# Kernel optimization log

Measured on AMD Instinct MI355X. Metric: run time of the kernel, lower is better.

## Reference

```python
import jax, jax.numpy as jnp
import numpy as np

B, S, H = 2, 2048, 2048           # batch, seq_len, hidden_size
NH, HD = 16, 128                  # num_heads, head_dim
ROPE_THETA = 10000.0


def _rope_cos_sin(seq_len, head_dim, dtype):
    # standard rotary embedding tables: [seq, head_dim]
    inv_freq = 1.0 / (ROPE_THETA ** (jnp.arange(0, head_dim, 2, dtype=jnp.float32) / head_dim))
    t = jnp.arange(seq_len, dtype=jnp.float32)
    freqs = jnp.einsum('s,d->sd', t, inv_freq)          # [S, HD/2]
    emb = jnp.concatenate([freqs, freqs], axis=-1)      # [S, HD]
    return jnp.cos(emb).astype(dtype), jnp.sin(emb).astype(dtype)


def _rotate_half(x):
    x1, x2 = jnp.split(x, 2, axis=-1)
    return jnp.concatenate([-x2, x1], axis=-1)


def _apply_rope(x, cos, sin):
    # x: [B, S, NH, HD]; cos/sin: [S, HD]
    return x * cos[None, :, None, :] + _rotate_half(x) * sin[None, :, None, :]


def setup_inputs() -> dict:
    key = jax.random.key(0)
    ks = jax.random.split(key, 10)
    hidden_states = jax.random.normal(ks[0], (B, S, H), dtype=jnp.float32)
    # causal mask: 1.0 where attention is disallowed (k > q), matching mask * -1e9 usage
    mask = jnp.triu(jnp.ones((S, S), dtype=jnp.float32), k=1)[None, None, :, :]
    mask = jnp.broadcast_to(mask, (B, 1, S, S))
    xav = 1.0 / np.sqrt(H)
    Wq = jax.random.uniform(ks[1], (H, NH, HD), jnp.float32, -xav, xav)
    Wk = jax.random.uniform(ks[2], (H, NH, HD), jnp.float32, -xav, xav)
    Wv = jax.random.uniform(ks[3], (H, NH, HD), jnp.float32, -xav, xav)
    Wo = jax.random.uniform(ks[4], (NH, HD, H), jnp.float32, -xav, xav)
    bq = jnp.zeros((NH, HD), jnp.float32)
    bk = jnp.zeros((NH, HD), jnp.float32)
    bv = jnp.zeros((NH, HD), jnp.float32)
    bo = jnp.zeros((H,), jnp.float32)
    return {"hidden_states": hidden_states, "mask": mask, "Wq": Wq, "bq": bq,
            "Wk": Wk, "bk": bk, "Wv": Wv, "bv": bv, "Wo": Wo, "bo": bo}


def reference(hidden_states, mask, Wq, bq, Wk, bk, Wv, bv, Wo, bo):
    dtype = hidden_states.dtype
    scale = 1.0 / jnp.sqrt(jnp.asarray(HD, dtype))
    # q/k/v projections: DenseGeneral hidden -> (heads, head_dim)
    q = jnp.einsum('bsh,bhd->bsnd'.replace('bhd', 'hnd'), hidden_states, Wq) + bq  # [B,S,NH,HD]
    k = jnp.einsum('bsh,hnd->bsnd', hidden_states, Wk) + bk
    v = jnp.einsum('bsh,hnd->bsnd', hidden_states, Wv) + bv
    cos, sin = _rope_cos_sin(hidden_states.shape[1], HD, dtype)
    q = _apply_rope(q, cos, sin)
    k = _apply_rope(k, cos, sin)
    # [B,NH,S,HD]
    q, k, v = (x.transpose(0, 2, 1, 3) for x in (q, k, v))
    attn_scores = jnp.einsum('bhqd,bhkd->bhqk', q, k) * scale
    attn_scores = attn_scores + mask * (-1e9)           # mask broadcasts over heads
    probs = jax.nn.softmax(attn_scores, axis=-1)
    attn_output = jnp.einsum('bhqk,bhkd->bhqd', probs, v)
    attn_output = attn_output.transpose(0, 2, 1, 3)      # [B,S,NH,HD]
    return jnp.einsum('bsnd,ndh->bsh', attn_output, Wo) + bo
```

## Files before the change

kernel.cpp:

```cpp
#include <hip/hip_runtime.h>
#include <hip/hip_bf16.h>

#define B_ 2
#define S_ 2048
#define H_ 2048
#define NH_ 16
#define HD_ 128
#define M_ (B_*S_)

typedef unsigned short u16;
typedef unsigned int u32;
typedef __attribute__((ext_vector_type(8))) short bhalf8_t;
typedef __attribute__((ext_vector_type(4))) float fx4_t;

__device__ __forceinline__ float bf2f(u16 v) {
    unsigned u = ((unsigned)v) << 16;
    return __builtin_bit_cast(float, u);
}
__device__ __forceinline__ u16 f2bf(float f) {
    unsigned u = __builtin_bit_cast(unsigned, f);
    unsigned r = u + 0x7fffu + ((u >> 16) & 1u);
    return (u16)(r >> 16);
}
__device__ __forceinline__ u16 f2bf_trunc(float f) {
    return (u16)(__builtin_bit_cast(unsigned, f) >> 16);
}
__device__ __forceinline__ void gload_lds16(const u16* g, u16* l) {
    __builtin_amdgcn_global_load_lds(
        (const __attribute__((address_space(1))) u32*)g,
        (__attribute__((address_space(3))) u32*)l, 16, 0, 0);
}
#define ASM_BAR()    __asm__ volatile("s_barrier" ::: "memory")
#define WAIT_VM0()   __asm__ volatile("s_waitcnt vmcnt(0)" ::: "memory")
#define WAIT_VM6()   __asm__ volatile("s_waitcnt vmcnt(6)" ::: "memory")
#define WAIT_LGKM0() __asm__ volatile("s_waitcnt lgkmcnt(0)" ::: "memory")

__global__ __launch_bounds__(256) void cvt_bf16_k(const float* __restrict__ in,
                                                  u16* __restrict__ out) {
    int i = blockIdx.x * 256 + threadIdx.x;
    float4 v = ((const float4*)in)[i];
    ushort4 o;
    o.x = f2bf(v.x); o.y = f2bf(v.y); o.z = f2bf(v.z); o.w = f2bf(v.w);
    ((ushort4*)out)[i] = o;
}

__global__ __launch_bounds__(256) void transpose_cvt4_k(const float* __restrict__ s0,
                                                        const float* __restrict__ s1,
                                                        const float* __restrict__ s2,
                                                        const float* __restrict__ s3,
                                                        u16* __restrict__ out) {
    const float* in = blockIdx.z == 0 ? s0 : blockIdx.z == 1 ? s1
                    : blockIdx.z == 2 ? s2 : s3;
    u16* dst = out + (size_t)blockIdx.z * H_ * H_;
    __shared__ u16 tile[64][65];
    int k0 = blockIdx.y * 64, n0 = blockIdx.x * 64;
    int t = threadIdx.x;
    for (int i = 0; i < 16; i++) {
        int idx = t + i * 256;
        int r = idx >> 6, c = idx & 63;
        tile[r][c] = f2bf(in[(size_t)(k0 + r) * H_ + n0 + c]);
    }
    __syncthreads();
    for (int i = 0; i < 16; i++) {
        int idx = t + i * 256;
        int r = idx >> 6, c = idx & 63;
        dst[(size_t)(n0 + r) * H_ + k0 + c] = tile[c][r];
    }
}

__global__ __launch_bounds__(512, 2) void gemm_qkv_tb(const u16* __restrict__ A,
                                                      const u16* __restrict__ Bt,
                                                      const float* __restrict__ bq,
                                                      const float* __restrict__ bk,
                                                      const float* __restrict__ bv,
                                                      u16* __restrict__ qh,
                                                      u16* __restrict__ kh,
                                                      u16* __restrict__ vT) {
    const int Ksz = H_;
    __shared__ u16 smA[3 * 8192];
    __shared__ u16 smB[3 * 16384];
    int t = threadIdx.x;
    int wave = t >> 6, lane = t & 63;
    int lr = lane & 15, lq = lane >> 4;
    int m0 = blockIdx.y * 128, n0 = blockIdx.x * 256;
    int wm = (wave >> 2) * 64, wn = (wave & 3) * 64;

    fx4_t acc[4][4];
#pragma unroll
    for (int i = 0; i < 4; i++)
        for (int j = 0; j < 4; j++)
            acc[i][j] = (fx4_t){0.f, 0.f, 0.f, 0.f};

    auto stageA = [&](int buf, int k0) {
        u16* dst = smA + buf * 8192;
#pragma unroll
        for (int i = 0; i < 2; i++) {
            int c = t + i * 512;
            int r = c >> 3, g = (c & 7) ^ (r & 7);
            gload_lds16(&A[(size_t)(m0 + r) * Ksz + k0 + g * 8], dst + (size_t)c * 8);
        }
    };
    auto stageB = [&](int buf, int k0) {
        u16* dst = smB + buf * 16384;
#pragma unroll
        for (int i = 0; i < 4; i++) {
            int c = t + i * 512;
            int r = c >> 3, g = (c & 7) ^ (r & 7);
            gload_lds16(&Bt[(size_t)(n0 + r) * Ksz + k0 + g * 8], dst + (size_t)c * 8);
        }
    };

    const int NT = Ksz / 64;
    stageA(0, 0);  stageB(0, 0);
    stageA(1, 64); stageB(1, 64);
    WAIT_VM6();
    ASM_BAR();

    for (int kt = 0; kt < NT; kt++) {
        int cur = kt % 3;
        const u16* Ab = smA + cur * 8192;
        const u16* Bb = smB + cur * 16384;
        bhalf8_t bfr[8];
        bhalf8_t afr[2][2];

#pragma unroll
        for (int nj = 0; nj < 4; nj++)
            for (int ks = 0; ks < 2; ks++) {
                int row = wn + nj * 16 + lr;
                bfr[nj * 2 + ks] = *(const bhalf8_t*)
                    &Bb[(((size_t)row << 3) + ((ks * 4 + lq) ^ (lr & 7))) * 8];
            }
#pragma unroll
        for (int mi2 = 0; mi2 < 2; mi2++)
            for (int ks = 0; ks < 2; ks++) {
                int row = wm + mi2 * 16 + lr;
                afr[mi2][ks] = *(const bhalf8_t*)
                    &Ab[(((size_t)row << 3) + ((ks * 4 + lq) ^ (lr & 7))) * 8];
            }
        if (kt + 2 < NT) {
            int nb = (kt + 2) % 3;
            stageA(nb, (kt + 2) * 64);
            stageB(nb, (kt + 2) * 64);
        }
        ASM_BAR();
        WAIT_LGKM0();
        __builtin_amdgcn_sched_barrier(0);
        __builtin_amdgcn_s_setprio(1);
#pragma unroll
        for (int mi2 = 0; mi2 < 2; mi2++)
            for (int nj = 0; nj < 4; nj++)
                for (int ks = 0; ks < 2; ks++)
                    acc[mi2][nj] = __builtin_amdgcn_mfma_f32_16x16x32_bf16(
                        afr[mi2][ks], bfr[nj * 2 + ks], acc[mi2][nj], 0, 0, 0);
        __builtin_amdgcn_s_setprio(0);
        ASM_BAR();

#pragma unroll
        for (int mi2 = 0; mi2 < 2; mi2++)
            for (int ks = 0; ks < 2; ks++) {
                int row = wm + (2 + mi2) * 16 + lr;
                afr[mi2][ks] = *(const bhalf8_t*)
                    &Ab[(((size_t)row << 3) + ((ks * 4 + lq) ^ (lr & 7))) * 8];
            }
        if (kt + 2 < NT) WAIT_VM6();
        else            WAIT_VM0();
        ASM_BAR();
        WAIT_LGKM0();
        __builtin_amdgcn_sched_barrier(0);
        __builtin_amdgcn_s_setprio(1);
#pragma unroll
        for (int mi2 = 0; mi2 < 2; mi2++)
            for (int nj = 0; nj < 4; nj++)
                for (int ks = 0; ks < 2; ks++)
                    acc[2 + mi2][nj] = __builtin_amdgcn_mfma_f32_16x16x32_bf16(
                        afr[mi2][ks], bfr[nj * 2 + ks], acc[2 + mi2][nj], 0, 0, 0);
        __builtin_amdgcn_s_setprio(0);
        ASM_BAR();
    }

    int which = n0 >> 11;
    const float* bias = which == 0 ? bq : which == 1 ? bk : bv;
#pragma unroll
    for (int mi = 0; mi < 4; mi++)
#pragma unroll
        for (int nj = 0; nj < 4; nj++) {
            int row0 = m0 + wm + mi * 16 + lq * 4;
            int cc = (n0 & 2047) + wn + nj * 16 + lr;
            float bvv = bias[cc];
            int bb = row0 >> 11, s = row0 & 2047;
            int hh = cc >> 7, d = cc & 127;
            if (which == 2) {
                ushort4 w;
                w.x = f2bf(acc[mi][nj][0] + bvv);
                w.y = f2bf(acc[mi][nj][1] + bvv);
                w.z = f2bf(acc[mi][nj][2] + bvv);
                w.w = f2bf(acc[mi][nj][3] + bvv);
                *(ushort4*)&vT[(((size_t)bb * NH_ + hh) * HD_ + d) * S_ + s] = w;
            } else {
                u16* dst = (which == 0 ? qh : kh);
                for (int r = 0; r < 4; r++)
                    dst[(((size_t)bb * NH_ + hh) * S_ + s + r) * HD_ + d] =
                        f2bf(acc[mi][nj][r] + bvv);
            }
        }
}

__global__ __launch_bounds__(256) void gemm_out(const u16* __restrict__ A,
                                                const u16* __restrict__ Bt,
                                                const float* __restrict__ bias,
                                                float* __restrict__ C) {
    const int Ksz = H_, Nsz = H_;
    __shared__ u16 As[128 * 64];
    __shared__ u16 Bs[128 * 64];
    int t = threadIdx.x;
    int wave = t >> 6, lane = t & 63;
    int lr = lane & 15, lq = lane >> 4;
    int m0 = blockIdx.y * 128, n0 = blockIdx.x * 128;
    int wm = (wave >> 1) * 64, wn = (wave & 1) * 64;

    fx4_t acc[4][4];
    for (int i = 0; i < 4; i++)
        for (int j = 0; j < 4; j++)
            acc[i][j] = (fx4_t){0.f, 0.f, 0.f, 0.f};

    for (int k0 = 0; k0 < Ksz; k0 += 64) {
        for (int i = 0; i < 4; i++) {
            int c = t + i * 256;
            int r = c >> 3, g = (c & 7) ^ (r & 7);
            gload_lds16(&A[(size_t)(m0 + r) * Ksz + k0 + g * 8], As + (size_t)c * 8);
            gload_lds16(&Bt[(size_t)(n0 + r) * Ksz + k0 + g * 8], Bs + (size_t)c * 8);
        }
        __syncthreads();
        for (int ds = 0; ds < 2; ds++) {
            bhalf8_t a[4], b[4];
            int cs = (ds * 4 + lq) ^ (lr & 7);
            for (int i = 0; i < 4; i++)
                a[i] = *(const bhalf8_t*)&As[(((wm + i * 16 + lr) << 3) + cs) * 8];
            for (int j = 0; j < 4; j++)
                b[j] = *(const bhalf8_t*)&Bs[(((wn + j * 16 + lr) << 3) + cs) * 8];
            for (int i = 0; i < 4; i++)
                for (int j = 0; j < 4; j++)
                    acc[i][j] = __builtin_amdgcn_mfma_f32_16x16x32_bf16(a[i], b[j], acc[i][j], 0, 0, 0);
        }
        __syncthreads();
    }
    for (int i = 0; i < 4; i++)
        for (int j = 0; j < 4; j++) {
            int row0 = m0 + wm + i * 16 + lq * 4;
            int col = n0 + wn + j * 16 + lr;
            float bvv = bias[col];
            for (int r = 0; r < 4; r++)
                C[(size_t)(row0 + r) * Nsz + col] = acc[i][j][r] + bvv;
        }
}

__global__ __launch_bounds__(256) void rope_k(u16* __restrict__ q, u16* __restrict__ k) {
    const float scale2 = 0.08838834764831845f * 1.44269504f;
    int idx = blockIdx.x * 256 + threadIdx.x;
    int i = idx & 63;
    int s = (idx >> 6) & 2047;
    int h = (idx >> 17) & 15;
    int b = idx >> 21;
    float inv = exp2f((float)i * (-13.287712379549449f / 64.0f));
    float ang = (float)s * inv;
    float sn, c;
    sincosf(ang, &sn, &c);
    size_t base = (((size_t)b * NH_ + h) * S_ + s) * HD_ + i;
    {
        float x1 = bf2f(q[base]), x2 = bf2f(q[base + 64]);
        q[base]      = f2bf((x1 * c - x2 * sn) * scale2);
        q[base + 64] = f2bf((x2 * c + x1 * sn) * scale2);
    }
    {
        float x1 = bf2f(k[base]), x2 = bf2f(k[base + 64]);
        k[base]      = f2bf(x1 * c - x2 * sn);
        k[base + 64] = f2bf(x2 * c + x1 * sn);
    }
}

#define PROW2 40
__global__ __launch_bounds__(256, 2) void flash_k(const u16* __restrict__ qh,
                                                  const u16* __restrict__ kh,
                                                  const u16* __restrict__ vT,
                                                  u16* __restrict__ attn) {
    __shared__ u16 sm[2 * 8192 + 2 * 8192 + 4 * 32 * PROW2];
    u16* KsB = sm;
    u16* VsB = sm + 16384;
    u16* Ps  = sm + 32768;

    int t = threadIdx.x, wave = t >> 6, lane = t & 63;
    int lr = lane & 15, lq = lane >> 4;
    int h = blockIdx.y, b = blockIdx.z;
    int ti = (b == 0) ? ((int)gridDim.x - 1 - (int)blockIdx.x) : (int)blockIdx.x;
    int q0 = ti * 128;

    const u16* kbase = kh + ((size_t)b * NH_ + h) * S_ * HD_;
    const u16* vbase = vT + ((size_t)b * NH_ + h) * HD_ * S_;
    u16* Pw = Ps + wave * 32 * PROW2;

    bhalf8_t aq[2][4];
#pragma unroll
    for (int rg = 0; rg < 2; rg++) {
        const u16* qrow =
            qh + (((size_t)b * NH_ + h) * S_ + q0 + wave * 32 + rg * 16 + lr) * HD_;
#pragma unroll
        for (int ds = 0; ds < 4; ds++)
            aq[rg][ds] = *(const bhalf8_t*)&qrow[ds * 32 + lq * 8];
    }

    float m_i[2][4], l_i[2][4];
    fx4_t acc_o[2][8];
#pragma unroll
    for (int rg = 0; rg < 2; rg++)
        for (int r = 0; r < 4; r++) { m_i[rg][r] = -INFINITY; l_i[rg][r] = 0.f; }
#pragma unroll
    for (int rg = 0; rg < 2; rg++)
        for (int dt = 0; dt < 8; dt++) acc_o[rg][dt] = (fx4_t){0.f, 0.f, 0.f, 0.f};

    bhalf8_t bones;
#pragma unroll
    for (int j = 0; j < 8; j++) bones[j] = (short)0x3F80;

    auto stageK = [&](int buf, int k0) {
        u16* dst = KsB + buf * 8192;
#pragma unroll
        for (int i = 0; i < 4; i++) {
            int c = t + i * 256;
            int r = c >> 4, g = (c & 15) ^ (r & 15);
            gload_lds16(&kbase[(size_t)(k0 + r) * HD_ + g * 8], dst + (size_t)c * 8);
        }
    };
    auto stageV = [&](int buf, int k0) {
        u16* dst = VsB + buf * 8192;
#pragma unroll
        for (int i = 0; i < 4; i++) {
            int c = t + i * 256;
            int r = c >> 3, g = (c & 7) ^ (r & 7);
            gload_lds16(&vbase[(size_t)r * S_ + k0 + g * 8], dst + (size_t)c * 8);
        }
    };

    int nkb = q0 / 64 + 2;
    stageK(0, 0);
    stageV(0, 0);
    for (int kbi = 0; kbi < nkb; kbi++) {
        int cur = kbi & 1;
        int k0 = kbi * 64;
        __syncthreads();
        if (kbi + 1 < nkb) {
            stageK(cur ^ 1, k0 + 64);
            stageV(cur ^ 1, k0 + 64);
        }
        const u16* Kc = KsB + cur * 8192;
        const u16* Vc = VsB + cur * 8192;

        bool active = (k0 <= q0 + wave * 32 + 31);

        fx4_t sacc[2][4];
        float alpha[2][4];
        if (active) {
#pragma unroll
            for (int rg = 0; rg < 2; rg++)
                for (int nt = 0; nt < 4; nt++)
                    sacc[rg][nt] = (fx4_t){0.f, 0.f, 0.f, 0.f};
            __builtin_amdgcn_s_setprio(1);
#pragma unroll
            for (int nt = 0; nt < 4; nt++) {
                int r = nt * 16 + lr;
#pragma unroll
                for (int ds = 0; ds < 4; ds++) {
                    bhalf8_t bk = *(const bhalf8_t*)&Kc[((r << 4) + ((ds * 4 + lq) ^ lr)) * 8];
                    sacc[0][nt] = __builtin_amdgcn_mfma_f32_16x16x32_bf16(aq[0][ds], bk, sacc[0][nt], 0, 0, 0);
                    sacc[1][nt] = __builtin_amdgcn_mfma_f32_16x16x32_bf16(aq[1][ds], bk, sacc[1][nt], 0, 0, 0);
                }
            }
            __builtin_amdgcn_s_setprio(0);

            if (kbi >= nkb - 2) {
#pragma unroll
                for (int rg = 0; rg < 2; rg++)
                    for (int nt = 0; nt < 4; nt++)
                        for (int r = 0; r < 4; r++) {
                            int kpos = k0 + nt * 16 + lr;
                            int qpos = q0 + wave * 32 + rg * 16 + lq * 4 + r;
                            if (kpos > qpos) sacc[rg][nt][r] = -1e30f;
                        }
            }

#pragma unroll
            for (int rg = 0; rg < 2; rg++) {
                float rmax[4];
#pragma unroll
                for (int r = 0; r < 4; r++)
                    rmax[r] = fmaxf(fmaxf(sacc[rg][0][r], sacc[rg][1][r]),
                                    fmaxf(sacc[rg][2][r], sacc[rg][3][r]));
#pragma unroll
                for (int off = 1; off < 16; off <<= 1)
                    for (int r = 0; r < 4; r++)
                        rmax[r] = fmaxf(rmax[r], __shfl_xor(rmax[r], off, 64));
#pragma unroll
                for (int r = 0; r < 4; r++) {
                    float mn = fmaxf(m_i[rg][r], rmax[r]);
                    alpha[rg][r] = exp2f(m_i[rg][r] - mn);
                    m_i[rg][r] = mn;
#pragma unroll
                    for (int nt = 0; nt < 4; nt++)
                        sacc[rg][nt][r] = exp2f(sacc[rg][nt][r] - mn);
                    l_i[rg][r] *= alpha[rg][r];
                }
#pragma unroll
                for (int dt = 0; dt < 8; dt++)
                    for (int r = 0; r < 4; r++) acc_o[rg][dt][r] *= alpha[rg][r];
            }

            fx4_t ls[2];
            ls[0] = (fx4_t){0.f, 0.f, 0.f, 0.f};
            ls[1] = (fx4_t){0.f, 0.f, 0.f, 0.f};
#pragma unroll
            for (int p = 0; p < 2; p++) {
#pragma unroll
                for (int rg = 0; rg < 2; rg++)
                    for (int nt2 = 0; nt2 < 2; nt2++)
                        for (int r = 0; r < 4; r++)
                            Pw[(rg * 16 + lq * 4 + r) * PROW2 + nt2 * 16 + lr] =
                                f2bf_trunc(sacc[rg][p * 2 + nt2][r]);
                __asm__ volatile("s_waitcnt lgkmcnt(0)" ::: "memory");
                bhalf8_t ap0 = *(const bhalf8_t*)&Pw[lr * PROW2 + lq * 8];
                bhalf8_t ap1 = *(const bhalf8_t*)&Pw[(16 + lr) * PROW2 + lq * 8];
                __builtin_amdgcn_s_setprio(1);
#pragma unroll
                for (int dt = 0; dt < 8; dt++) {
                    int r = dt * 16 + lr;
                    bhalf8_t bv = *(const bhalf8_t*)&Vc[((r << 3) + ((p * 4 + lq) ^ (lr & 7))) * 8];
                    acc_o[0][dt] = __builtin_amdgcn_mfma_f32_16x16x32_bf16(ap0, bv, acc_o[0][dt], 0, 0, 0);
                    acc_o[1][dt] = __builtin_amdgcn_mfma_f32_16x16x32_bf16(ap1, bv, acc_o[1][dt], 0, 0, 0);
                }
                ls[0] = __builtin_amdgcn_mfma_f32_16x16x32_bf16(ap0, bones, ls[0], 0, 0, 0);
                ls[1] = __builtin_amdgcn_mfma_f32_16x16x32_bf16(ap1, bones, ls[1], 0, 0, 0);
                __builtin_amdgcn_s_setprio(0);
            }
#pragma unroll
            for (int rg = 0; rg < 2; rg++)
                for (int r = 0; r < 4; r++) l_i[rg][r] += ls[rg][r];
        }
    }

#pragma unroll
    for (int rg = 0; rg < 2; rg++) {
        float rl[4];
#pragma unroll
        for (int r = 0; r < 4; r++) rl[r] = 1.f / l_i[rg][r];
#pragma unroll
        for (int dt = 0; dt < 8; dt++)
            for (int r = 0; r < 4; r++) {
                size_t row = (size_t)(b * S_ + q0 + wave * 32 + rg * 16 + lq * 4 + r);
                attn[(row * NH_ + h) * HD_ + dt * 16 + lr] = f2bf(acc_o[rg][dt][r] * rl[r]);
            }
    }
}

extern "C" void kernel_launch(void* const* d_in, const int* in_sizes, int n_in,
                              void* d_out, int out_size, void* d_ws, size_t ws_size,
                              hipStream_t stream) {
    const float* hs = (const float*)d_in[0];
    const float* Wq = (const float*)d_in[2];
    const float* bq = (const float*)d_in[3];
    const float* Wk = (const float*)d_in[4];
    const float* bk = (const float*)d_in[5];
    const float* Wv = (const float*)d_in[6];
    const float* bv = (const float*)d_in[7];
    const float* Wo = (const float*)d_in[8];
    const float* bo = (const float*)d_in[9];
    float* out = (float*)d_out;

    u16* ws   = (u16*)d_ws;
    size_t WW = (size_t)H_ * H_;
    size_t AC = (size_t)M_ * H_;
    u16* hsb  = ws;
    u16* Wall = hsb + AC;
    u16* WoT  = Wall + 3 * WW;
    u16* qh   = WoT + WW;
    u16* kh   = qh + AC;
    u16* vT   = kh + AC;
    u16* attn = vT + AC;

    dim3 tb(256);

    cvt_bf16_k<<<dim3(AC / (256 * 4)), tb, 0, stream>>>(hs, hsb);

    transpose_cvt4_k<<<dim3(32, 32, 4), tb, 0, stream>>>(Wq, Wk, Wv, Wo, Wall);

    gemm_qkv_tb<<<dim3(3 * H_ / 256, M_ / 128), dim3(512), 0, stream>>>(hsb, Wall,
                                                                        bq, bk, bv,
                                                                        qh, kh, vT);

    rope_k<<<dim3((B_ * NH_ * S_ * 64) / 256), tb, 0, stream>>>(qh, kh);

    flash_k<<<dim3(S_ / 128, NH_, B_), tb, 0, stream>>>(qh, kh, vT, attn);

    gemm_out<<<dim3(H_ / 128, M_ / 128), tb, 0, stream>>>(attn, WoT, bo, out);
}
```

Before: 441.3 us.

## Simplify QKV GEMM main loop to one barrier per k-tile

Replaces the two-phase ping-pong loop (split A fragments, four barriers, setprio and sched_barrier per k-tile) with a single barrier per iteration. Each iteration waits for the current tile, issues prefetch of tile k+2, loads all A and B fragments, then runs all MFMAs. This cuts barrier and wait overhead and lets the compiler interleave LDS reads with MFMAs. It gives up explicit wave priority control and raises fragment register pressure.

```diff
diff --git a/kernel.cpp b/kernel.cpp
--- a/kernel.cpp
+++ b/kernel.cpp
@@ -33,7 +33,6 @@
 #define ASM_BAR()    __asm__ volatile("s_barrier" ::: "memory")
 #define WAIT_VM0()   __asm__ volatile("s_waitcnt vmcnt(0)" ::: "memory")
 #define WAIT_VM6()   __asm__ volatile("s_waitcnt vmcnt(6)" ::: "memory")
-#define WAIT_LGKM0() __asm__ volatile("s_waitcnt lgkmcnt(0)" ::: "memory")
 
 __global__ __launch_bounds__(256) void cvt_bf16_k(const float* __restrict__ in,
                                                   u16* __restrict__ out) {
@@ -113,69 +112,43 @@
     const int NT = Ksz / 64;
     stageA(0, 0);  stageB(0, 0);
     stageA(1, 64); stageB(1, 64);
-    WAIT_VM6();
-    ASM_BAR();
 
     for (int kt = 0; kt < NT; kt++) {
         int cur = kt % 3;
         const u16* Ab = smA + cur * 8192;
         const u16* Bb = smB + cur * 16384;
-        bhalf8_t bfr[8];
-        bhalf8_t afr[2][2];
-
-#pragma unroll
-        for (int nj = 0; nj < 4; nj++)
-            for (int ks = 0; ks < 2; ks++) {
-                int row = wn + nj * 16 + lr;
-                bfr[nj * 2 + ks] = *(const bhalf8_t*)
-                    &Bb[(((size_t)row << 3) + ((ks * 4 + lq) ^ (lr & 7))) * 8];
-            }
-#pragma unroll
-        for (int mi2 = 0; mi2 < 2; mi2++)
-            for (int ks = 0; ks < 2; ks++) {
-                int row = wm + mi2 * 16 + lr;
-                afr[mi2][ks] = *(const bhalf8_t*)
-                    &Ab[(((size_t)row << 3) + ((ks * 4 + lq) ^ (lr & 7))) * 8];
-            }
+
+        if (kt == NT - 1) WAIT_VM0();
+        else              WAIT_VM6();
+        ASM_BAR();
+
         if (kt + 2 < NT) {
             int nb = (kt + 2) % 3;
             stageA(nb, (kt + 2) * 64);
             stageB(nb, (kt + 2) * 64);
         }
-        ASM_BAR();
-        WAIT_LGKM0();
-        __builtin_amdgcn_sched_barrier(0);
-        __builtin_amdgcn_s_setprio(1);
-#pragma unroll
-        for (int mi2 = 0; mi2 < 2; mi2++)
+
+        bhalf8_t afr[4][2], bfr[4][2];
+#pragma unroll
+        for (int nj = 0; nj < 4; nj++)
+            for (int ks = 0; ks < 2; ks++) {
+                int row = wn + nj * 16 + lr;
+                bfr[nj][ks] = *(const bhalf8_t*)
+                    &Bb[(((size_t)row << 3) + ((ks * 4 + lq) ^ (lr & 7))) * 8];
+            }
+#pragma unroll
+        for (int mi = 0; mi < 4; mi++)
+            for (int ks = 0; ks < 2; ks++) {
+                int row = wm + mi * 16 + lr;
+                afr[mi][ks] = *(const bhalf8_t*)
+                    &Ab[(((size_t)row << 3) + ((ks * 4 + lq) ^ (lr & 7))) * 8];
+            }
+#pragma unroll
+        for (int mi = 0; mi < 4; mi++)
             for (int nj = 0; nj < 4; nj++)
                 for (int ks = 0; ks < 2; ks++)
-                    acc[mi2][nj] = __builtin_amdgcn_mfma_f32_16x16x32_bf16(
-                        afr[mi2][ks], bfr[nj * 2 + ks], acc[mi2][nj], 0, 0, 0);
-        __builtin_amdgcn_s_setprio(0);
-        ASM_BAR();
-
-#pragma unroll
-        for (int mi2 = 0; mi2 < 2; mi2++)
-            for (int ks = 0; ks < 2; ks++) {
-                int row = wm + (2 + mi2) * 16 + lr;
-                afr[mi2][ks] = *(const bhalf8_t*)
-                    &Ab[(((size_t)row << 3) + ((ks * 4 + lq) ^ (lr & 7))) * 8];
-            }
-        if (kt + 2 < NT) WAIT_VM6();
-        else            WAIT_VM0();
-        ASM_BAR();
-        WAIT_LGKM0();
-        __builtin_amdgcn_sched_barrier(0);
-        __builtin_amdgcn_s_setprio(1);
-#pragma unroll
-        for (int mi2 = 0; mi2 < 2; mi2++)
-            for (int nj = 0; nj < 4; nj++)
-                for (int ks = 0; ks < 2; ks++)
-                    acc[2 + mi2][nj] = __builtin_amdgcn_mfma_f32_16x16x32_bf16(
-                        afr[mi2][ks], bfr[nj * 2 + ks], acc[2 + mi2][nj], 0, 0, 0);
-        __builtin_amdgcn_s_setprio(0);
-        ASM_BAR();
+                    acc[mi][nj] = __builtin_amdgcn_mfma_f32_16x16x32_bf16(
+                        afr[mi][ks], bfr[nj][ks], acc[mi][nj], 0, 0, 0);
     }
 
     int which = n0 >> 11;
```

New measurement: 465.5 us. 5.5% more time.
